# Kernel optimization log

Measured on AMD Instinct MI355X. Metric: run time of the kernel, lower is better.

## Reference

```python
import jax, jax.numpy as jnp
import numpy as np

N_NODES = 50000
N_EDGES = 1600000
N_GRAPHS = 512
IN_SIZE = 44
HIDDEN = 256
CONV_NUMS = 3


def setup_inputs() -> dict:
    key = jax.random.key(0)
    ks = jax.random.split(key, 10)
    h = jax.random.normal(ks[0], (N_NODES, IN_SIZE), dtype=jnp.float32)
    src = jax.random.randint(ks[1], (N_EDGES,), 0, N_NODES)
    dst = jax.random.randint(ks[2], (N_EDGES,), 0, N_NODES)
    graph_ids = jnp.sort(jax.random.randint(ks[3], (N_NODES,), 0, N_GRAPHS))
    # learned params (kaiming-ish scale)
    W_proj = jax.random.normal(ks[4], (IN_SIZE, HIDDEN), dtype=jnp.float32) * (2.0 / IN_SIZE) ** 0.5
    b_proj = jnp.zeros((HIDDEN,), dtype=jnp.float32)
    W_lin = jax.random.normal(ks[5], (HIDDEN, HIDDEN), dtype=jnp.float32) * (2.0 / HIDDEN) ** 0.5
    b_lin = jnp.zeros((HIDDEN,), dtype=jnp.float32)
    W_out = jax.random.normal(ks[6], (HIDDEN * CONV_NUMS, HIDDEN), dtype=jnp.float32) * (2.0 / (HIDDEN * CONV_NUMS)) ** 0.5
    b_out = jnp.zeros((HIDDEN,), dtype=jnp.float32)
    return {"h": h, "src": src, "dst": dst, "graph_ids": graph_ids,
            "W_proj": W_proj, "b_proj": b_proj, "W_lin": W_lin, "b_lin": b_lin,
            "W_out": W_out, "b_out": b_out}


def reference(h, src, dst, graph_ids, W_proj, b_proj, W_lin, b_lin, W_out, b_out):
    # initial projection
    h = h @ W_proj + b_proj  # [N, HIDDEN]
    # in-degree for mean aggregation (nodes with 0 in-edges get 0 aggregate)
    ones_e = jnp.ones((src.shape[0],), dtype=h.dtype)
    deg = jax.ops.segment_sum(ones_e, dst, num_segments=N_NODES)  # [N]
    inv_deg = jnp.where(deg > 0, 1.0 / jnp.maximum(deg, 1.0), 0.0)[:, None]
    outs = []
    for _ in range(CONV_NUMS):
        # DGL GINConv(mean, eps=0): h' = linear(h + mean_{u in N(v)} h_u)
        agg = jax.ops.segment_sum(h[src], dst, num_segments=N_NODES) * inv_deg
        h = (h + agg) @ W_lin + b_lin  # shared linear across layers
        outs.append(h)
    res = jnp.concatenate(outs, axis=1) @ W_out + b_out  # [N, HIDDEN]
    # dgl.mean_nodes: per-graph mean readout
    cnt = jax.ops.segment_sum(jnp.ones((N_NODES,), dtype=res.dtype), graph_ids, num_segments=N_GRAPHS)
    g_sum = jax.ops.segment_sum(res, graph_ids, num_segments=N_GRAPHS)
    return g_sum / jnp.maximum(cnt, 1.0)[:, None]
```

## Files before the change

kernel.cpp:

```cpp
#include <hip/hip_runtime.h>
#include <hip/hip_fp8.h>

#define N_NODES   50000
#define N_EDGES   1600000
#define N_GRAPHS  512
#define IN_SIZE   44
#define HIDDEN    256
#define CONV_NUMS 3
#define NBK       ((N_NODES + 255) / 256)
#define XK        48

typedef __attribute__((ext_vector_type(8))) short short8v;
typedef __attribute__((ext_vector_type(4))) float f32x4;

__device__ __forceinline__ float bf2f(unsigned short u) {
    return __uint_as_float(((unsigned int)u) << 16);
}
__device__ __forceinline__ unsigned short f2bf(float f) {
    unsigned int u = __float_as_uint(f);
    unsigned int r = (u + 0x7fffu + ((u >> 16) & 1u)) >> 16;
    return (unsigned short)r;
}

#if __has_builtin(__builtin_amdgcn_cvt_f32_fp8)
template <int SEL>
__device__ __forceinline__ float fp8tof(unsigned int w) {
    return __builtin_amdgcn_cvt_f32_fp8((int)w, SEL);
}
#else
template <int SEL>
__device__ __forceinline__ float fp8tof(unsigned int w) {
    __hip_fp8_e4m3 q;
    q.__x = (__hip_fp8_storage_t)((w >> (SEL * 8)) & 0xff);
    return (float)q;
}
#endif

#if __has_builtin(__builtin_amdgcn_cvt_pk_fp8_f32)
__device__ __forceinline__ unsigned int pk4fp8(float f0, float f1, float f2, float f3) {
    int lo = __builtin_amdgcn_cvt_pk_fp8_f32(f0, f1, 0, false);
    return (unsigned int)__builtin_amdgcn_cvt_pk_fp8_f32(f2, f3, lo, true);
}
#else
__device__ __forceinline__ unsigned int pk4fp8(float f0, float f1, float f2, float f3) {
    __hip_fp8_e4m3 a(f0), b(f1), c(f2), d(f3);
    return (unsigned int)a.__x | ((unsigned int)b.__x << 8) |
           ((unsigned int)c.__x << 16) | ((unsigned int)d.__x << 24);
}
#endif

__global__ __launch_bounds__(256) void k_passA(const int* __restrict__ dst,
                                               const int* __restrict__ gid,
                                               int* __restrict__ bucket_cnt,
                                               int* __restrict__ gcnt) {
    __shared__ int hb[NBK];
    __shared__ int hg[N_GRAPHS];
    int tid = threadIdx.x;
    for (int i = tid; i < NBK; i += 256) hb[i] = 0;
    for (int i = tid; i < N_GRAPHS; i += 256) hg[i] = 0;
    __syncthreads();
    int t = blockIdx.x * 256 + tid;
    int stride = gridDim.x * 256;
    for (int e = t; e < N_EDGES; e += stride) atomicAdd(&hb[dst[e] >> 8], 1);
    for (int v = t; v < N_NODES; v += stride) atomicAdd(&hg[gid[v]], 1);
    __syncthreads();
    for (int i = tid; i < NBK; i += 256) if (hb[i]) atomicAdd(&bucket_cnt[i], hb[i]);
    for (int i = tid; i < N_GRAPHS; i += 256) if (hg[i]) atomicAdd(&gcnt[i], hg[i]);
}

__global__ void k_bscan(const int* __restrict__ bucket_cnt, int* __restrict__ bucket_base,
                        int* __restrict__ bucket_cursor, int* __restrict__ row_ptr) {
    __shared__ int s[256];
    int t = threadIdx.x;
    int v = (t < NBK) ? bucket_cnt[t] : 0;
    s[t] = v;
    __syncthreads();
    for (int off = 1; off < 256; off <<= 1) {
        int a = (t >= off) ? s[t - off] : 0;
        __syncthreads();
        s[t] += a;
        __syncthreads();
    }
    if (t < NBK) {
        int base = s[t] - v;
        bucket_base[t] = base;
        bucket_cursor[t] = base;
    }
    if (t == 0) {
        bucket_base[NBK] = N_EDGES;
        row_ptr[N_NODES] = N_EDGES;
    }
}

#define BCH 4096
__global__ __launch_bounds__(256) void k_passB(const int* __restrict__ src,
                                               const int* __restrict__ dst,
                                               int* __restrict__ bucket_cursor,
                                               int* __restrict__ pairs) {
    __shared__ int hist[NBK];
    __shared__ int excl[NBK];
    __shared__ int cur[NBK];
    __shared__ int gbase[NBK];
    __shared__ int lp[BCH];
    __shared__ int sc[256];
    int tid = threadIdx.x;
    int e0 = blockIdx.x * BCH;
    int cnt = min(BCH, N_EDGES - e0);
    for (int i = tid; i < NBK; i += 256) hist[i] = 0;
    __syncthreads();
    for (int i = tid; i < cnt; i += 256) atomicAdd(&hist[dst[e0 + i] >> 8], 1);
    __syncthreads();
    int hv = (tid < NBK) ? hist[tid] : 0;
    sc[tid] = hv;
    __syncthreads();
    for (int off = 1; off < 256; off <<= 1) {
        int a = (tid >= off) ? sc[tid - off] : 0;
        __syncthreads();
        sc[tid] += a;
        __syncthreads();
    }
    if (tid < NBK) {
        excl[tid] = sc[tid] - hv;
        cur[tid]  = sc[tid] - hv;
    }
    __syncthreads();
    for (int i = tid; i < cnt; i += 256) {
        int d = dst[e0 + i];
        int b = d >> 8;
        int pos = atomicAdd(&cur[b], 1);
        lp[pos] = (b << 24) | ((d & 255) << 16) | src[e0 + i];
    }
    __syncthreads();
    if (tid < NBK && hist[tid] > 0)
        gbase[tid] = atomicAdd(&bucket_cursor[tid], hist[tid]);
    __syncthreads();
    for (int i = tid; i < cnt; i += 256) {
        int p = lp[i];
        int b = (p >> 24) & 0xff;
        pairs[gbase[b] + (i - excl[b])] = p;
    }
}

__global__ __launch_bounds__(256) void k_passC(const int* __restrict__ pairs,
                                               const int* __restrict__ bucket_base,
                                               int* __restrict__ row_ptr,
                                               unsigned short* __restrict__ colu) {
    __shared__ int hist[256];
    __shared__ int cur[256];
    __shared__ int sc[256];
    int b = blockIdx.x;
    int tid = threadIdx.x;
    int v0 = b << 8;
    int e0 = bucket_base[b], e1 = bucket_base[b + 1];
    hist[tid] = 0;
    __syncthreads();
    for (int i = e0 + tid; i < e1; i += 256) atomicAdd(&hist[(pairs[i] >> 16) & 0xff], 1);
    __syncthreads();
    int hv = hist[tid];
    sc[tid] = hv;
    __syncthreads();
    for (int off = 1; off < 256; off <<= 1) {
        int a = (tid >= off) ? sc[tid - off] : 0;
        __syncthreads();
        sc[tid] += a;
        __syncthreads();
    }
    int base = e0 + sc[tid] - hv;
    int v = v0 + tid;
    if (v < N_NODES) row_ptr[v] = base;
    cur[tid] = base;
    __syncthreads();
    for (int i = e0 + tid; i < e1; i += 256) {
        int p = pairs[i];
        int pos = atomicAdd(&cur[(p >> 16) & 0xff], 1);
        colu[pos] = (unsigned short)(p & 0xffff);
    }
}

__global__ __launch_bounds__(256) void k_prep(const float* __restrict__ Wl,
                                              const float* __restrict__ Wproj,
                                              const float* __restrict__ X,
                                              unsigned short* __restrict__ WlPack,
                                              unsigned short* __restrict__ WprojPack,
                                              unsigned short* __restrict__ Xb) {
    int b = blockIdx.x;
    int tid = threadIdx.x;
    if (b < 32) {
        int i = b * 256 + tid;
        int kg = i >> 8, n = i & 255;
        short8v v;
#pragma unroll
        for (int j = 0; j < 8; j++) v[j] = (short)f2bf(Wl[(kg * 8 + j) * HIDDEN + n]);
        *(short8v*)(WlPack + (size_t)(kg * 256 + n) * 8) = v;
    } else if (b < 40) {
        int i = (b - 32) * 256 + tid;
        int kg = i >> 8, n = i & 255;
        short8v v;
#pragma unroll
        for (int j = 0; j < 8; j++) {
            int k = kg * 8 + j;
            v[j] = (k < IN_SIZE) ? (short)f2bf(Wproj[k * HIDDEN + n]) : (short)0;
        }
        *(short8v*)(WprojPack + (size_t)(kg * 256 + n) * 8) = v;
    } else {
        const int TOT = N_NODES * XK;
        int id0 = (b - 40) * 2048 + tid;
#pragma unroll
        for (int j = 0; j < 8; j++) {
            int id = id0 + j * 256;
            if (id < TOT) {
                int row = id / XK, c = id % XK;
                Xb[id] = (c < IN_SIZE) ? f2bf(X[row * IN_SIZE + c]) : (unsigned short)0;
            }
        }
    }
}

#define TLS 264
#define K1S 72
__global__ __launch_bounds__(512, 8) void k_layer1(const unsigned short* __restrict__ Xb,
                                                   const int* __restrict__ row_ptr,
                                                   const unsigned short* __restrict__ colu,
                                                   const unsigned short* __restrict__ WprojPack,
                                                   const float* __restrict__ bp,
                                                   const unsigned short* __restrict__ WlPack,
                                                   const float* __restrict__ bl,
                                                   const int* __restrict__ gid,
                                                   unsigned short* __restrict__ hout,
                                                   unsigned char* __restrict__ hout8,
                                                   float* __restrict__ GsumL) {
    __shared__ unsigned short tl[64 * TLS];
    unsigned short* tl1 = tl;
    __shared__ float bpm[64];
    __shared__ int gl[64];
    int tid = threadIdx.x;
    int w = tid >> 6, lane = tid & 63, quad = lane >> 4, l16 = lane & 15;
    int m0 = blockIdx.x * 64;

    for (int rr = 0; rr < 8; rr++) {
        int r = w * 8 + rr;
        int v = m0 + r;
        float a0 = 0.f, a1 = 0.f;
        float val = 0.f;
        float mul = 1.f;
        if (v < N_NODES) {
            int s = row_ptr[v], e = row_ptr[v + 1];
            if (lane < XK) {
                int i = s;
                for (; i + 8 <= e; i += 8) {
                    int u0 = colu[i],     u1 = colu[i + 1];
                    int u2 = colu[i + 2], u3 = colu[i + 3];
                    int u4 = colu[i + 4], u5 = colu[i + 5];
                    int u6 = colu[i + 6], u7 = colu[i + 7];
                    float t0 = bf2f(Xb[u0 * XK + lane]);
                    float t1 = bf2f(Xb[u1 * XK + lane]);
                    float t2 = bf2f(Xb[u2 * XK + lane]);
                    float t3 = bf2f(Xb[u3 * XK + lane]);
                    float t4 = bf2f(Xb[u4 * XK + lane]);
                    float t5 = bf2f(Xb[u5 * XK + lane]);
                    float t6 = bf2f(Xb[u6 * XK + lane]);
                    float t7 = bf2f(Xb[u7 * XK + lane]);
                    a0 += (t0 + t1) + (t2 + t3);
                    a1 += (t4 + t5) + (t6 + t7);
                }
                for (; i + 2 <= e; i += 2) {
                    a0 += bf2f(Xb[colu[i] * XK + lane]);
                    a1 += bf2f(Xb[colu[i + 1] * XK + lane]);
                }
                if (i < e) a0 += bf2f(Xb[colu[i] * XK + lane]);
            }
            float inv = 0.f;
            if (e > s) { inv = 1.0f / (float)(e - s); mul = 2.f; }
            float self = (lane < XK) ? bf2f(Xb[(size_t)v * XK + lane]) : 0.f;
            val = self + inv * (a0 + a1);
        }
        tl1[r * K1S + lane] = (lane < XK) ? f2bf(val) : (unsigned short)0;
        if (lane == 0) bpm[r] = mul;
    }
    if (tid < 64) gl[tid] = (m0 + tid < N_NODES) ? gid[m0 + tid] : -1;
    __syncthreads();

    int n0 = w * 32;
    f32x4 acc[4][2];
#pragma unroll
    for (int mt = 0; mt < 4; mt++) {
        acc[mt][0] = (f32x4){0.f, 0.f, 0.f, 0.f};
        acc[mt][1] = (f32x4){0.f, 0.f, 0.f, 0.f};
    }
#pragma unroll
    for (int ks = 0; ks < 2; ks++) {
        int kg = ks * 4 + quad;
        short8v bfr0 = *(const short8v*)(WprojPack + (size_t)(kg * 256 + n0 + l16) * 8);
        short8v bfr1 = *(const short8v*)(WprojPack + (size_t)(kg * 256 + n0 + 16 + l16) * 8);
#pragma unroll
        for (int mt = 0; mt < 4; mt++) {
            short8v afr = *(const short8v*)(tl1 + (mt * 16 + l16) * K1S + ks * 32 + quad * 8);
            acc[mt][0] = __builtin_amdgcn_mfma_f32_16x16x32_bf16(afr, bfr0, acc[mt][0], 0, 0, 0);
            acc[mt][1] = __builtin_amdgcn_mfma_f32_16x16x32_bf16(afr, bfr1, acc[mt][1], 0, 0, 0);
        }
    }
    __syncthreads();
#pragma unroll
    for (int nt = 0; nt < 2; nt++) {
        int colg = n0 + nt * 16 + l16;
        float bb = bp[colg];
#pragma unroll
        for (int mt = 0; mt < 4; mt++)
#pragma unroll
            for (int r = 0; r < 4; r++) {
                int row = mt * 16 + quad * 4 + r;
                tl[row * TLS + colg] = f2bf(acc[mt][nt][r] + bb * bpm[row]);
            }
    }
    __syncthreads();

#pragma unroll
    for (int mt = 0; mt < 4; mt++) {
        acc[mt][0] = (f32x4){0.f, 0.f, 0.f, 0.f};
        acc[mt][1] = (f32x4){0.f, 0.f, 0.f, 0.f};
    }
#pragma unroll
    for (int ks = 0; ks < 8; ks++) {
        int kg = ks * 4 + quad;
        short8v bfr0 = *(const short8v*)(WlPack + (size_t)(kg * 256 + n0 + l16) * 8);
        short8v bfr1 = *(const short8v*)(WlPack + (size_t)(kg * 256 + n0 + 16 + l16) * 8);
#pragma unroll
        for (int mt = 0; mt < 4; mt++) {
            short8v afr = *(const short8v*)(tl + (mt * 16 + l16) * TLS + ks * 32 + quad * 8);
            acc[mt][0] = __builtin_amdgcn_mfma_f32_16x16x32_bf16(afr, bfr0, acc[mt][0], 0, 0, 0);
            acc[mt][1] = __builtin_amdgcn_mfma_f32_16x16x32_bf16(afr, bfr1, acc[mt][1], 0, 0, 0);
        }
    }
    __syncthreads();

#pragma unroll
    for (int nt = 0; nt < 2; nt++) {
        int colg = n0 + nt * 16 + l16;
        float bb = bl[colg];
#pragma unroll
        for (int mt = 0; mt < 4; mt++)
#pragma unroll
            for (int r = 0; r < 4; r++)
                tl[(mt * 16 + quad * 4 + r) * TLS + colg] = f2bf(acc[mt][nt][r] + bb);
    }
    __syncthreads();

    for (int i = tid; i < 64 * 64; i += 512) {
        int r = i >> 6, c4 = i & 63;
        int v = m0 + r;
        if (v < N_NODES) {
            ushort4 q = *(ushort4*)(tl + r * TLS + c4 * 4);
            ((ushort4*)hout)[(size_t)v * 64 + c4] = q;
            ((unsigned int*)hout8)[(size_t)v * 64 + c4] =
                pk4fp8(bf2f(q.x), bf2f(q.y), bf2f(q.z), bf2f(q.w));
        }
    }
    {
        int c = tid & 255;
        int r0 = (tid >> 8) * 32;
        float a2 = 0.f;
        int curg = gl[r0];
        for (int r = r0; r < r0 + 32; r++) {
            int g = gl[r];
            if (g < 0) break;
            if (g != curg) {
                atomicAdd(&GsumL[curg * HIDDEN + c], a2);
                a2 = 0.f;
                curg = g;
            }
            a2 += bf2f(tl[r * TLS + c]);
        }
        if (curg >= 0) atomicAdd(&GsumL[curg * HIDDEN + c], a2);
    }
}

__global__ __launch_bounds__(512, 8) void k_layer(const unsigned short* __restrict__ h,
                                                  const unsigned char* __restrict__ h8,
                                                  const int* __restrict__ row_ptr,
                                                  const unsigned short* __restrict__ colu,
                                                  const unsigned short* __restrict__ Wpack,
                                                  const float* __restrict__ bias,
                                                  const int* __restrict__ gid,
                                                  unsigned short* __restrict__ hout,
                                                  unsigned char* __restrict__ hout8,
                                                  int write8,
                                                  float* __restrict__ GsumL) {
    __shared__ unsigned short tl[64 * TLS];
    __shared__ int gl[64];
    int tid = threadIdx.x;
    int w = tid >> 6, lane = tid & 63, quad = lane >> 4, l16 = lane & 15;
    int m0 = blockIdx.x * 64;

    const unsigned int* h8v = (const unsigned int*)h8;
    const ushort4* hv = (const ushort4*)h;
    for (int rr = 0; rr < 8; rr++) {
        int r = w * 8 + rr;
        int v = m0 + r;
        float a0 = 0.f, a1 = 0.f, a2 = 0.f, a3 = 0.f;
        if (v < N_NODES) {
            int s = row_ptr[v], e = row_ptr[v + 1];
            int i = s;
            for (; i + 8 <= e; i += 8) {
                int u0 = colu[i],     u1 = colu[i + 1];
                int u2 = colu[i + 2], u3 = colu[i + 3];
                int u4 = colu[i + 4], u5 = colu[i + 5];
                int u6 = colu[i + 6], u7 = colu[i + 7];
                unsigned int p0 = h8v[(size_t)u0 * 64 + lane];
                unsigned int p1 = h8v[(size_t)u1 * 64 + lane];
                unsigned int p2 = h8v[(size_t)u2 * 64 + lane];
                unsigned int p3 = h8v[(size_t)u3 * 64 + lane];
                unsigned int p4 = h8v[(size_t)u4 * 64 + lane];
                unsigned int p5 = h8v[(size_t)u5 * 64 + lane];
                unsigned int p6 = h8v[(size_t)u6 * 64 + lane];
                unsigned int p7 = h8v[(size_t)u7 * 64 + lane];
                a0 += (fp8tof<0>(p0) + fp8tof<0>(p1)) + (fp8tof<0>(p2) + fp8tof<0>(p3))
                    + (fp8tof<0>(p4) + fp8tof<0>(p5)) + (fp8tof<0>(p6) + fp8tof<0>(p7));
                a1 += (fp8tof<1>(p0) + fp8tof<1>(p1)) + (fp8tof<1>(p2) + fp8tof<1>(p3))
                    + (fp8tof<1>(p4) + fp8tof<1>(p5)) + (fp8tof<1>(p6) + fp8tof<1>(p7));
                a2 += (fp8tof<2>(p0) + fp8tof<2>(p1)) + (fp8tof<2>(p2) + fp8tof<2>(p3))
                    + (fp8tof<2>(p4) + fp8tof<2>(p5)) + (fp8tof<2>(p6) + fp8tof<2>(p7));
                a3 += (fp8tof<3>(p0) + fp8tof<3>(p1)) + (fp8tof<3>(p2) + fp8tof<3>(p3))
                    + (fp8tof<3>(p4) + fp8tof<3>(p5)) + (fp8tof<3>(p6) + fp8tof<3>(p7));
            }
            for (; i + 4 <= e; i += 4) {
                int u0 = colu[i], u1 = colu[i + 1], u2 = colu[i + 2], u3 = colu[i + 3];
                unsigned int p0 = h8v[(size_t)u0 * 64 + lane];
                unsigned int p1 = h8v[(size_t)u1 * 64 + lane];
                unsigned int p2 = h8v[(size_t)u2 * 64 + lane];
                unsigned int p3 = h8v[(size_t)u3 * 64 + lane];
                a0 += (fp8tof<0>(p0) + fp8tof<0>(p1)) + (fp8tof<0>(p2) + fp8tof<0>(p3));
                a1 += (fp8tof<1>(p0) + fp8tof<1>(p1)) + (fp8tof<1>(p2) + fp8tof<1>(p3));
                a2 += (fp8tof<2>(p0) + fp8tof<2>(p1)) + (fp8tof<2>(p2) + fp8tof<2>(p3));
                a3 += (fp8tof<3>(p0) + fp8tof<3>(p1)) + (fp8tof<3>(p2) + fp8tof<3>(p3));
            }
            for (; i < e; i++) {
                unsigned int p = h8v[(size_t)colu[i] * 64 + lane];
                a0 += fp8tof<0>(p); a1 += fp8tof<1>(p);
                a2 += fp8tof<2>(p); a3 += fp8tof<3>(p);
            }
            float inv = (e > s) ? 1.0f / (float)(e - s) : 0.0f;
            ushort4 hs = hv[(size_t)v * 64 + lane];
            a0 = bf2f(hs.x) + inv * a0;
            a1 = bf2f(hs.y) + inv * a1;
            a2 = bf2f(hs.z) + inv * a2;
            a3 = bf2f(hs.w) + inv * a3;
        }
        ushort4 o;
        o.x = f2bf(a0); o.y = f2bf(a1); o.z = f2bf(a2); o.w = f2bf(a3);
        *(ushort4*)(tl + r * TLS + lane * 4) = o;
    }
    if (tid < 64) gl[tid] = (m0 + tid < N_NODES) ? gid[m0 + tid] : -1;
    __syncthreads();

    int n0 = w * 32;
    f32x4 acc[4][2];
#pragma unroll
    for (int mt = 0; mt < 4; mt++) {
        acc[mt][0] = (f32x4){0.f, 0.f, 0.f, 0.f};
        acc[mt][1] = (f32x4){0.f, 0.f, 0.f, 0.f};
    }
#pragma unroll
    for (int ks = 0; ks < 8; ks++) {
        int kg = ks * 4 + quad;
        short8v bfr0 = *(const short8v*)(Wpack + (size_t)(kg * 256 + n0 + l16) * 8);
        short8v bfr1 = *(const short8v*)(Wpack + (size_t)(kg * 256 + n0 + 16 + l16) * 8);
#pragma unroll
        for (int mt = 0; mt < 4; mt++) {
            short8v afr = *(const short8v*)(tl + (mt * 16 + l16) * TLS + ks * 32 + quad * 8);
            acc[mt][0] = __builtin_amdgcn_mfma_f32_16x16x32_bf16(afr, bfr0, acc[mt][0], 0, 0, 0);
            acc[mt][1] = __builtin_amdgcn_mfma_f32_16x16x32_bf16(afr, bfr1, acc[mt][1], 0, 0, 0);
        }
    }
    __syncthreads();

#pragma unroll
    for (int nt = 0; nt < 2; nt++) {
        int colg = n0 + nt * 16 + l16;
        float bb = bias[colg];
#pragma unroll
        for (int mt = 0; mt < 4; mt++)
#pragma unroll
            for (int r = 0; r < 4; r++)
                tl[(mt * 16 + quad * 4 + r) * TLS + colg] = f2bf(acc[mt][nt][r] + bb);
    }
    __syncthreads();

    for (int i = tid; i < 64 * 64; i += 512) {
        int r = i >> 6, c4 = i & 63;
        int v = m0 + r;
        if (v < N_NODES) {
            ushort4 q = *(ushort4*)(tl + r * TLS + c4 * 4);
            ((ushort4*)hout)[(size_t)v * 64 + c4] = q;
            if (write8)
                ((unsigned int*)hout8)[(size_t)v * 64 + c4] =
                    pk4fp8(bf2f(q.x), bf2f(q.y), bf2f(q.z), bf2f(q.w));
        }
    }
    {
        int c = tid & 255;
        int r0 = (tid >> 8) * 32;
        float a2 = 0.f;
        int curg = gl[r0];
        for (int r = r0; r < r0 + 32; r++) {
            int g = gl[r];
            if (g < 0) break;
            if (g != curg) {
                atomicAdd(&GsumL[curg * HIDDEN + c], a2);
                a2 = 0.f;
                curg = g;
            }
            a2 += bf2f(tl[r * TLS + c]);
        }
        if (curg >= 0) atomicAdd(&GsumL[curg * HIDDEN + c], a2);
    }
}

__global__ __launch_bounds__(256) void k_out(const float* __restrict__ Gsum,
                                             const int* __restrict__ gcnt,
                                             const float* __restrict__ Wout,
                                             const float* __restrict__ bout,
                                             float* __restrict__ out) {
    int g = blockIdx.x;
    int c = threadIdx.x;
    __shared__ float gm[HIDDEN * CONV_NUMS];
    float invc = 1.0f / fmaxf((float)gcnt[g], 1.0f);
    for (int i = c; i < HIDDEN * CONV_NUMS; i += 256) {
        int l = i >> 8;
        int k = i & 255;
        gm[i] = Gsum[(size_t)l * N_GRAPHS * HIDDEN + g * HIDDEN + k] * invc;
    }
    __syncthreads();
    float acc = bout[c];
    const float4* gm4 = (const float4*)gm;
    for (int k0 = 0; k0 < HIDDEN * CONV_NUMS; k0 += 4) {
        float4 gv = gm4[k0 >> 2];
        acc += gv.x * Wout[(k0 + 0) * HIDDEN + c];
        acc += gv.y * Wout[(k0 + 1) * HIDDEN + c];
        acc += gv.z * Wout[(k0 + 2) * HIDDEN + c];
        acc += gv.w * Wout[(k0 + 3) * HIDDEN + c];
    }
    out[g * HIDDEN + c] = acc;
}

extern "C" void kernel_launch(void* const* d_in, const int* in_sizes, int n_in,
                              void* d_out, int out_size, void* d_ws, size_t ws_size,
                              hipStream_t stream) {
    const float* X    = (const float*)d_in[0];
    const int*   src  = (const int*)d_in[1];
    const int*   dst  = (const int*)d_in[2];
    const int*   gid  = (const int*)d_in[3];
    const float* Wp   = (const float*)d_in[4];
    const float* bp   = (const float*)d_in[5];
    const float* Wl   = (const float*)d_in[6];
    const float* bl   = (const float*)d_in[7];
    const float* Wout = (const float*)d_in[8];
    const float* bout = (const float*)d_in[9];
    float* out = (float*)d_out;

    char* ws = (char*)d_ws;
    size_t off = 0;
    auto alloc = [&](size_t bytes) {
        char* p = ws + off;
        off += (bytes + 255) & ~size_t(255);
        return p;
    };
    unsigned short* h         = (unsigned short*)alloc(sizeof(short) * N_NODES * HIDDEN);
    unsigned short* t         = (unsigned short*)alloc(sizeof(short) * N_NODES * HIDDEN);
    unsigned char*  h8a       = (unsigned char*)alloc((size_t)N_NODES * HIDDEN);
    unsigned char*  h8b       = (unsigned char*)alloc((size_t)N_NODES * HIDDEN);
    unsigned short* WlPack    = (unsigned short*)alloc(sizeof(short) * HIDDEN * HIDDEN);
    unsigned short* WprojPack = (unsigned short*)alloc(sizeof(short) * 8 * 256 * 8);
    unsigned short* Xb        = (unsigned short*)alloc(sizeof(short) * N_NODES * XK);
    int*   pairs   = (int*)alloc(sizeof(int) * N_EDGES);
    unsigned short* colu = (unsigned short*)alloc(sizeof(short) * N_EDGES);
    int*   row_ptr = (int*)alloc(sizeof(int) * (N_NODES + 1));
    int*   bucket_base   = (int*)alloc(sizeof(int) * (NBK + 1));
    int*   bucket_cursor = (int*)alloc(sizeof(int) * NBK);
    char*  zero0 = ws + off;
    int*   bucket_cnt = (int*)alloc(sizeof(int) * NBK);
    int*   gcnt       = (int*)alloc(sizeof(int) * N_GRAPHS);
    float* Gsum       = (float*)alloc(sizeof(float) * CONV_NUMS * N_GRAPHS * HIDDEN);
    size_t zero_bytes = (size_t)((char*)(Gsum + CONV_NUMS * N_GRAPHS * HIDDEN) - zero0);

    hipMemsetAsync(zero0, 0, zero_bytes, stream);

    k_passA<<<512, 256, 0, stream>>>(dst, gid, bucket_cnt, gcnt);
    k_bscan<<<1, 256, 0, stream>>>(bucket_cnt, bucket_base, bucket_cursor, row_ptr);
    k_passB<<<(N_EDGES + BCH - 1) / BCH, 256, 0, stream>>>(src, dst, bucket_cursor, pairs);
    {
        const int TOT = N_NODES * XK;
        int ncast = (TOT + 2047) / 2048;
        k_prep<<<40 + ncast, 256, 0, stream>>>(Wl, Wp, X, WlPack, WprojPack, Xb);
    }
    k_passC<<<NBK, 256, 0, stream>>>(pairs, bucket_base, row_ptr, colu);

    k_layer1<<<(N_NODES + 63) / 64, 512, 0, stream>>>(
        Xb, row_ptr, colu, WprojPack, bp, WlPack, bl, gid, h, h8a, Gsum);

    k_layer<<<(N_NODES + 63) / 64, 512, 0, stream>>>(
        h, h8a, row_ptr, colu, WlPack, bl, gid, t, h8b, 1,
        Gsum + (size_t)1 * N_GRAPHS * HIDDEN);

    k_layer<<<(N_NODES + 63) / 64, 512, 0, stream>>>(
        t, h8b, row_ptr, colu, WlPack, bl, gid, h, h8a, 0,
        Gsum + (size_t)2 * N_GRAPHS * HIDDEN);

    k_out<<<N_GRAPHS, 256, 0, stream>>>(Gsum, gcnt, Wout, bout, out);
}
```

Before: 366.2 us.

## Balance per-wave edge work in layer kernels, gather FP8 input features

Each 64-row block now caches its row_ptr slice in shared memory and splits rows among the 8 waves by binary search on edge counts, so waves get roughly equal numbers of edges instead of a fixed 8 rows each. The first layer's neighbor gather reads an FP8 copy of the input features, produced in the prep kernel, instead of BF16, halving gather bytes. The passB chunk size is also doubled. The FP8 input gather lowers precision of the first-layer aggregation, and rows that straddle a split boundary rely on the binary search assigning each row to exactly one wave.

Measured after the change: 372.9 us. No clear change (+1.8%).

```diff
diff --git a/kernel.cpp b/kernel.cpp
--- a/kernel.cpp
+++ b/kernel.cpp
@@ -48,6 +48,10 @@
            ((unsigned int)c.__x << 16) | ((unsigned int)d.__x << 24);
 }
 #endif
+
+__device__ __forceinline__ unsigned char f2fp8(float f) {
+    return (unsigned char)(pk4fp8(f, 0.f, 0.f, 0.f) & 0xff);
+}
 
 __global__ __launch_bounds__(256) void k_passA(const int* __restrict__ dst,
                                                const int* __restrict__ gid,
@@ -92,7 +96,7 @@
     }
 }
 
-#define BCH 4096
+#define BCH 8192
 __global__ __launch_bounds__(256) void k_passB(const int* __restrict__ src,
                                                const int* __restrict__ dst,
                                                int* __restrict__ bucket_cursor,
@@ -182,7 +186,8 @@
                                               const float* __restrict__ X,
                                               unsigned short* __restrict__ WlPack,
                                               unsigned short* __restrict__ WprojPack,
-                                              unsigned short* __restrict__ Xb) {
+                                              unsigned short* __restrict__ Xb,
+                                              unsigned char* __restrict__ Xb8) {
     int b = blockIdx.x;
     int tid = threadIdx.x;
     if (b < 32) {
@@ -210,15 +215,29 @@
             int id = id0 + j * 256;
             if (id < TOT) {
                 int row = id / XK, c = id % XK;
-                Xb[id] = (c < IN_SIZE) ? f2bf(X[row * IN_SIZE + c]) : (unsigned short)0;
-            }
-        }
-    }
+                float val = (c < IN_SIZE) ? X[row * IN_SIZE + c] : 0.f;
+                Xb[id]  = f2bf(val);
+                Xb8[id] = f2fp8(val);
+            }
+        }
+    }
+}
+
+__device__ __forceinline__ int rsplit(const int* rp, int s0, int len, int k) {
+    if (k >= 8) return 64;
+    int t = s0 + (int)(((long long)len * k) >> 3);
+    int lo = 0, hi = 64;
+    while (lo < hi) {
+        int mid = (lo + hi) >> 1;
+        if (rp[mid] < t) lo = mid + 1; else hi = mid;
+    }
+    return lo;
 }
 
 #define TLS 264
 #define K1S 72
 __global__ __launch_bounds__(512, 8) void k_layer1(const unsigned short* __restrict__ Xb,
+                                                   const unsigned char* __restrict__ Xb8,
                                                    const int* __restrict__ row_ptr,
                                                    const unsigned short* __restrict__ colu,
                                                    const unsigned short* __restrict__ WprojPack,
@@ -233,18 +252,24 @@
     unsigned short* tl1 = tl;
     __shared__ float bpm[64];
     __shared__ int gl[64];
+    __shared__ int rp[65];
     int tid = threadIdx.x;
     int w = tid >> 6, lane = tid & 63, quad = lane >> 4, l16 = lane & 15;
     int m0 = blockIdx.x * 64;
 
-    for (int rr = 0; rr < 8; rr++) {
-        int r = w * 8 + rr;
+    if (tid < 65) rp[tid] = row_ptr[min(m0 + tid, N_NODES)];
+    if (tid < 64) gl[tid] = (m0 + tid < N_NODES) ? gid[m0 + tid] : -1;
+    __syncthreads();
+    int s0 = rp[0], len = rp[64] - s0;
+    int rlo = rsplit(rp, s0, len, w), rhi = rsplit(rp, s0, len, w + 1);
+
+    for (int r = rlo; r < rhi; r++) {
         int v = m0 + r;
         float a0 = 0.f, a1 = 0.f;
         float val = 0.f;
         float mul = 1.f;
         if (v < N_NODES) {
-            int s = row_ptr[v], e = row_ptr[v + 1];
+            int s = rp[r], e = rp[r + 1];
             if (lane < XK) {
                 int i = s;
                 for (; i + 8 <= e; i += 8) {
@@ -252,22 +277,22 @@
                     int u2 = colu[i + 2], u3 = colu[i + 3];
                     int u4 = colu[i + 4], u5 = colu[i + 5];
                     int u6 = colu[i + 6], u7 = colu[i + 7];
-                    float t0 = bf2f(Xb[u0 * XK + lane]);
-                    float t1 = bf2f(Xb[u1 * XK + lane]);
-                    float t2 = bf2f(Xb[u2 * XK + lane]);
-                    float t3 = bf2f(Xb[u3 * XK + lane]);
-                    float t4 = bf2f(Xb[u4 * XK + lane]);
-                    float t5 = bf2f(Xb[u5 * XK + lane]);
-                    float t6 = bf2f(Xb[u6 * XK + lane]);
-                    float t7 = bf2f(Xb[u7 * XK + lane]);
-                    a0 += (t0 + t1) + (t2 + t3);
-                    a1 += (t4 + t5) + (t6 + t7);
+                    unsigned int t0 = Xb8[u0 * XK + lane];
+                    unsigned int t1 = Xb8[u1 * XK + lane];
+                    unsigned int t2 = Xb8[u2 * XK + lane];
+                    unsigned int t3 = Xb8[u3 * XK + lane];
+                    unsigned int t4 = Xb8[u4 * XK + lane];
+                    unsigned int t5 = Xb8[u5 * XK + lane];
+                    unsigned int t6 = Xb8[u6 * XK + lane];
+                    unsigned int t7 = Xb8[u7 * XK + lane];
+                    a0 += (fp8tof<0>(t0) + fp8tof<0>(t1)) + (fp8tof<0>(t2) + fp8tof<0>(t3));
+                    a1 += (fp8tof<0>(t4) + fp8tof<0>(t5)) + (fp8tof<0>(t6) + fp8tof<0>(t7));
                 }
                 for (; i + 2 <= e; i += 2) {
-                    a0 += bf2f(Xb[colu[i] * XK + lane]);
-                    a1 += bf2f(Xb[colu[i + 1] * XK + lane]);
+                    a0 += fp8tof<0>((unsigned int)Xb8[colu[i] * XK + lane]);
+                    a1 += fp8tof<0>((unsigned int)Xb8[colu[i + 1] * XK + lane]);
                 }
-                if (i < e) a0 += bf2f(Xb[colu[i] * XK + lane]);
+                if (i < e) a0 += fp8tof<0>((unsigned int)Xb8[colu[i] * XK + lane]);
             }
             float inv = 0.f;
             if (e > s) { inv = 1.0f / (float)(e - s); mul = 2.f; }
@@ -277,7 +302,6 @@
         tl1[r * K1S + lane] = (lane < XK) ? f2bf(val) : (unsigned short)0;
         if (lane == 0) bpm[r] = mul;
     }
-    if (tid < 64) gl[tid] = (m0 + tid < N_NODES) ? gid[m0 + tid] : -1;
     __syncthreads();
 
     int n0 = w * 32;
@@ -387,18 +411,24 @@
                                                   float* __restrict__ GsumL) {
     __shared__ unsigned short tl[64 * TLS];
     __shared__ int gl[64];
+    __shared__ int rp[65];
     int tid = threadIdx.x;
     int w = tid >> 6, lane = tid & 63, quad = lane >> 4, l16 = lane & 15;
     int m0 = blockIdx.x * 64;
 
+    if (tid < 65) rp[tid] = row_ptr[min(m0 + tid, N_NODES)];
+    if (tid < 64) gl[tid] = (m0 + tid < N_NODES) ? gid[m0 + tid] : -1;
+    __syncthreads();
+    int s0 = rp[0], len = rp[64] - s0;
+    int rlo = rsplit(rp, s0, len, w), rhi = rsplit(rp, s0, len, w + 1);
+
     const unsigned int* h8v = (const unsigned int*)h8;
     const ushort4* hv = (const ushort4*)h;
-    for (int rr = 0; rr < 8; rr++) {
-        int r = w * 8 + rr;
+    for (int r = rlo; r < rhi; r++) {
         int v = m0 + r;
         float a0 = 0.f, a1 = 0.f, a2 = 0.f, a3 = 0.f;
         if (v < N_NODES) {
-            int s = row_ptr[v], e = row_ptr[v + 1];
+            int s = rp[r], e = rp[r + 1];
             int i = s;
             for (; i + 8 <= e; i += 8) {
                 int u0 = colu[i],     u1 = colu[i + 1];
@@ -449,7 +479,6 @@
         o.x = f2bf(a0); o.y = f2bf(a1); o.z = f2bf(a2); o.w = f2bf(a3);
         *(ushort4*)(tl + r * TLS + lane * 4) = o;
     }
-    if (tid < 64) gl[tid] = (m0 + tid < N_NODES) ? gid[m0 + tid] : -1;
     __syncthreads();
 
     int n0 = w * 32;
@@ -571,6 +600,7 @@
     unsigned short* WlPack    = (unsigned short*)alloc(sizeof(short) * HIDDEN * HIDDEN);
     unsigned short* WprojPack = (unsigned short*)alloc(sizeof(short) * 8 * 256 * 8);
     unsigned short* Xb        = (unsigned short*)alloc(sizeof(short) * N_NODES * XK);
+    unsigned char*  Xb8       = (unsigned char*)alloc((size_t)N_NODES * XK);
     int*   pairs   = (int*)alloc(sizeof(int) * N_EDGES);
     unsigned short* colu = (unsigned short*)alloc(sizeof(short) * N_EDGES);
     int*   row_ptr = (int*)alloc(sizeof(int) * (N_NODES + 1));
@@ -590,12 +620,12 @@
     {
         const int TOT = N_NODES * XK;
         int ncast = (TOT + 2047) / 2048;
-        k_prep<<<40 + ncast, 256, 0, stream>>>(Wl, Wp, X, WlPack, WprojPack, Xb);
+        k_prep<<<40 + ncast, 256, 0, stream>>>(Wl, Wp, X, WlPack, WprojPack, Xb, Xb8);
     }
     k_passC<<<NBK, 256, 0, stream>>>(pairs, bucket_base, row_ptr, colu);
 
     k_layer1<<<(N_NODES + 63) / 64, 512, 0, stream>>>(
-        Xb, row_ptr, colu, WprojPack, bp, WlPack, bl, gid, h, h8a, Gsum);
+        Xb, Xb8, row_ptr, colu, WprojPack, bp, WlPack, bl, gid, h, h8a, Gsum);
 
     k_layer<<<(N_NODES + 63) / 64, 512, 0, stream>>>(
         h, h8a, row_ptr, colu, WlPack, bl, gid, t, h8b, 1,
```
